# Optimization experiments

Hardware: AMD Instinct MI355X
Metric: run time of the kernel (lower is better)

The kernel has to match this reference:

```python
import jax, jax.numpy as jnp
import numpy as np

B, S, D, H = 2, 2048, 1024, 16
HD = D // H  # 64
ROPE_BASE = 10000.0


def _rope_tables(seq_len, head_dim):
    pos = jnp.arange(seq_len, dtype=jnp.float32)
    inv_freq = 1.0 / (ROPE_BASE ** (jnp.arange(0, head_dim, 2, dtype=jnp.float32) / head_dim))
    ang = pos[:, None] * inv_freq[None, :]            # [S, HD/2]
    emb = jnp.concatenate([ang, ang], axis=-1)        # [S, HD]
    return jnp.cos(emb), jnp.sin(emb)


def setup_inputs() -> dict:
    key = jax.random.key(0)
    k0, k1, k2 = jax.random.split(key, 3)
    x = jax.random.normal(k0, (B, S, D), dtype=jnp.float32)
    Wq = jax.random.normal(k1, (D, D), dtype=jnp.float32) * 0.02
    Wv = jax.random.normal(k2, (D, D), dtype=jnp.float32) * 0.02
    cos, sin = _rope_tables(S, HD)
    return {"x": x, "Wq": Wq, "Wv": Wv, "cos": cos, "sin": sin}


def _rotate_half(u):
    h = u.shape[-1] // 2
    return jnp.concatenate([-u[..., h:], u[..., :h]], axis=-1)


def reference(x, Wq, Wv, cos, sin):
    b, s, d = x.shape
    h, hd = H, d // H
    # NOTE: source module has xk = self.query(x) (key uses query weights) -- preserved.
    xq = (x @ Wq.T).reshape(b, s, h, hd)
    xk = (x @ Wq.T).reshape(b, s, h, hd)
    xv = (x @ Wv.T).reshape(b, s, h, hd)
    c = cos[None, :, None, :]  # [1,S,1,HD]
    sn = sin[None, :, None, :]
    q = xq * c + _rotate_half(xq) * sn
    k = xk * c + _rotate_half(xk) * sn
    q = q.transpose(0, 2, 1, 3)   # [B,H,S,HD]
    k = k.transpose(0, 2, 1, 3)
    v = xv.transpose(0, 2, 1, 3)
    scale = 1.0 / jnp.sqrt(jnp.asarray(hd, dtype=q.dtype))
    scores = jnp.einsum('bhqd,bhkd->bhqk', q, k) * scale  # [B,H,S,S]
    causal = jnp.tril(jnp.ones((s, s), dtype=bool))
    scores = jnp.where(causal[None, None, :, :], scores, jnp.finfo(scores.dtype).min)
    probs = jax.nn.softmax(scores, axis=-1)
    out = jnp.einsum('bhqk,bhkd->bhqd', probs, v)
    return out.transpose(0, 2, 1, 3).reshape(b, s, d)
```

## Files before the change

kernel.cpp:

```cpp
#include <hip/hip_runtime.h>


typedef float f32x4 __attribute__((ext_vector_type(4)));
typedef short s16x8 __attribute__((ext_vector_type(8)));

__device__ inline unsigned short f2bf(float f) {
  union { float f; unsigned u; } v; v.f = f;
  unsigned r = v.u + 0x7FFFu + ((v.u >> 16) & 1u);
  return (unsigned short)(r >> 16);
}

__device__ inline void gload16(const unsigned short* g, unsigned short* l) {
  __builtin_amdgcn_global_load_lds(
      (const __attribute__((address_space(1))) unsigned int*)g,
      (__attribute__((address_space(3))) unsigned int*)l, 16, 0, 0);
}

__global__ __launch_bounds__(256) void convert_all(
    const float* __restrict__ x, const float* __restrict__ wq,
    const float* __restrict__ wv, unsigned short* __restrict__ xb,
    unsigned short* __restrict__ wqb, unsigned short* __restrict__ wvb) {
  int i = blockIdx.x * 256 + threadIdx.x;
  const float* src; unsigned short* dst; int off;
  if (i < 1048576) { src = x; dst = xb; off = i; }
  else if (i < 1310720) { src = wq; dst = wqb; off = i - 1048576; }
  else { src = wv; dst = wvb; off = i - 1310720; }
  float4 v = ((const float4*)src)[off];
  ushort4 o;
  o.x = f2bf(v.x); o.y = f2bf(v.y); o.z = f2bf(v.z); o.w = f2bf(v.w);
  ((ushort4*)dst)[off] = o;
}

__global__ __launch_bounds__(256, 2) void qv_gemm(
    const unsigned short* __restrict__ A, const unsigned short* __restrict__ Wq,
    const unsigned short* __restrict__ Wv, const float* __restrict__ cosT,
    const float* __restrict__ sinT, unsigned short* __restrict__ Kf,
    unsigned short* __restrict__ Vf) {
  __shared__ unsigned short GS[2][2][128][64];
  int tid = threadIdx.x;
  int isq = blockIdx.x < 256;
  int b256 = blockIdx.x & 255;
  int bm = b256 & 31, bn = b256 >> 5;
  int w = tid >> 6, lane = tid & 63, lr = lane & 15, lg = lane >> 4;
  int wm = w >> 1, wn = w & 1;
  int l8 = lane >> 3, l7 = lane & 7;
  f32x4 acc[4][4] = {};

  const unsigned short* Wp = isq ? Wq : Wv;
  const unsigned short* srcbase =
      (w < 2) ? (A + bm * 128 * 1024) : (Wp + bn * 128 * 1024);
  int ab = w >> 1;

  auto stage = [&](int step) {
    int buf = step & 1, kt = step * 64;
#pragma unroll
    for (int i = 0; i < 8; ++i) {
      int rgrp = (w & 1) * 8 + i;
      int u = rgrp * 8 + l8;
      int ch = l7 ^ (u & 7);
      gload16(srcbase + u * 1024 + kt + ch * 8,
              (unsigned short*)&GS[buf][ab][rgrp * 8][0]);
    }
  };

  stage(0);
  for (int step = 0; step < 16; ++step) {
    int buf = step & 1;
    asm volatile("s_waitcnt vmcnt(0)" ::: "memory");
    __syncthreads();
    if (step + 1 < 16) stage(step + 1);
    s16x8 af[4][2], bfr[4][2];
#pragma unroll
    for (int mf = 0; mf < 4; ++mf)
#pragma unroll
      for (int kk = 0; kk < 2; ++kk)
        af[mf][kk] = *(const s16x8*)
            &GS[buf][0][wm * 64 + mf * 16 + lr][((kk * 4 + lg) ^ (lr & 7)) * 8];
#pragma unroll
    for (int nf = 0; nf < 4; ++nf)
#pragma unroll
      for (int kk = 0; kk < 2; ++kk)
        bfr[nf][kk] = *(const s16x8*)
            &GS[buf][1][wn * 64 + nf * 16 + lr][((kk * 4 + lg) ^ (lr & 7)) * 8];
#pragma unroll
    for (int mf = 0; mf < 4; ++mf)
#pragma unroll
      for (int nf = 0; nf < 4; ++nf)
#pragma unroll
        for (int kk = 0; kk < 2; ++kk)
          acc[mf][nf] = __builtin_amdgcn_mfma_f32_16x16x32_bf16(
              af[mf][kk], bfr[nf][kk], acc[mf][nf], 0, 0, 0);
  }

  int mBase = bm * 128 + wm * 64;
  int nBase = bn * 128 + wn * 64;
  if (isq) {
    __syncthreads();
    unsigned short* Lw = &GS[0][0][0][0] + w * (64 * 72);
    int wavebase = mBase;
    int bq = wavebase >> 11;
    int sbase = wavebase & 2047;
    int kt = sbase >> 6;
    int h = (nBase >> 6);
    int bh = bq * 16 + h;
#pragma unroll
    for (int mf = 0; mf < 4; ++mf)
#pragma unroll
      for (int j = 0; j < 4; ++j) {
        int sp = mf * 16 + 4 * lg + j;
        int s = sbase + sp;
#pragma unroll
        for (int nf = 0; nf < 4; ++nf) {
          int hd = nf * 16 + lr;
          float self = acc[mf][nf][j];
          float part = (nf < 2) ? -acc[mf][nf + 2][j] : acc[mf][nf - 2][j];
          float val = self * cosT[s * 64 + hd] + part * sinT[s * 64 + hd];
          Lw[sp * 72 + hd] = f2bf(val);
        }
      }
    asm volatile("s_waitcnt lgkmcnt(0)" ::: "memory");
    __builtin_amdgcn_sched_barrier(0);
    unsigned short* KfT = Kf + (size_t)(bh * 32 + kt) * 4096;
#pragma unroll
    for (int i = 0; i < 8; ++i) {
      int kk = i & 1, nfk = i >> 1;
      int lg2 = lane >> 4, lr2 = lane & 15;
      int sp = ((nfk >> 1) << 5) | ((lr2 >> 2) << 3) | ((nfk & 1) << 2) |
               (lr2 & 3);
      int c = kk * 4 + lg2;
      s16x8 vch = *(const s16x8*)&Lw[sp * 72 + c * 8];
      *(s16x8*)&KfT[(i * 64 + lane) * 8] = vch;
    }
  } else {
#pragma unroll
    for (int mf = 0; mf < 4; ++mf) {
      int m0 = mBase + mf * 16 + 4 * lg;
      int b = m0 >> 11, s0 = m0 & 2047;
      int kt = s0 >> 6, w0 = s0 & 63;
      int kkv = w0 >> 5, lg2 = (w0 >> 3) & 3, e0 = w0 & 7;
#pragma unroll
      for (int nf = 0; nf < 4; ++nf) {
        int col = nBase + nf * 16 + lr;
        int h = col >> 6;
        int bh = b * 16 + h;
        ushort4 pk;
        pk.x = f2bf(acc[mf][nf][0]); pk.y = f2bf(acc[mf][nf][1]);
        pk.z = f2bf(acc[mf][nf][2]); pk.w = f2bf(acc[mf][nf][3]);
        int idx = (((((bh * 32 + kt) * 4 + nf) * 2 + kkv) * 64) +
                   lg2 * 16 + lr) * 8 + e0;
        *(ushort4*)&Vf[idx] = pk;
      }
    }
  }
}

__global__ __launch_bounds__(256, 2) void attn(
    const unsigned short* __restrict__ Kf,
    const unsigned short* __restrict__ Vf,
    float* __restrict__ out) {
  __shared__ float MB[2][2][4][16][17];
  __shared__ float ML[2][2][2][16];
  const float SC = 0.125f * 1.44269504088896f;
  const float THR = 44.0f;
  int tid = threadIdx.x;
  int fid = blockIdx.x;
  int bh = 4 * (fid & 7) + ((fid >> 3) & 3);
  int qt = 31 - (fid >> 5);
  int w = tid >> 6, lane = tid & 63, lr = lane & 15, lg = lane >> 4;
  int q0 = qt * 64, qh = w >> 1, par = w & 1;

  const unsigned short* KfB = Kf + (size_t)bh * 32 * 4096;
  const unsigned short* VfB = Vf + (size_t)bh * 32 * 4096;

  s16x8 aq[2][2];
#pragma unroll
  for (int qs = 0; qs < 2; ++qs) {
    int qr = q0 + qh * 32 + 16 * qs + lr;
    int ktq = qr >> 6, w64 = qr & 63;
    int nfq = ((w64 >> 5) << 1) | ((w64 >> 2) & 1);
    int r31 = w64 & 31;
    int lr2 = ((r31 >> 3) << 2) | (r31 & 3);
#pragma unroll
    for (int kk = 0; kk < 2; ++kk)
      aq[qs][kk] = *(const s16x8*)
          &KfB[((((ktq * 4 + nfq) * 2 + kk) * 64) + lg * 16 + lr2) * 8];
  }

  f32x4 o[2][4] = {};
  float m_[2] = {-1e30f, -1e30f}, l_[2] = {0.f, 0.f};

  s16x8 kf[4][2], vf[4][2];
  auto loadK = [&](int kt) {
#pragma unroll
    for (int nf = 0; nf < 4; ++nf)
#pragma unroll
      for (int kk = 0; kk < 2; ++kk)
        kf[nf][kk] = *(const s16x8*)
            &KfB[(((kt * 4 + nf) * 2 + kk) * 64 + lane) * 8];
  };
  auto loadV = [&](int kt) {
#pragma unroll
    for (int nf = 0; nf < 4; ++nf)
#pragma unroll
      for (int kk = 0; kk < 2; ++kk)
        vf[nf][kk] = *(const s16x8*)
            &VfB[(((kt * 4 + nf) * 2 + kk) * 64 + lane) * 8];
  };

  int kt = par;
  bool active = kt <= qt;
  if (active) { loadK(kt); loadV(kt); }
  while (active) {
    f32x4 sa[2][4];
#pragma unroll
    for (int qs = 0; qs < 2; ++qs)
#pragma unroll
      for (int nf = 0; nf < 4; ++nf) sa[qs][nf] = (f32x4){0.f, 0.f, 0.f, 0.f};
#pragma unroll
    for (int kk = 0; kk < 2; ++kk)
#pragma unroll
      for (int nf = 0; nf < 4; ++nf)
#pragma unroll
        for (int qs = 0; qs < 2; ++qs)
          sa[qs][nf] = __builtin_amdgcn_mfma_f32_16x16x32_bf16(
              kf[nf][kk], aq[qs][kk], sa[qs][nf], 0, 0, 0);

    int ktn = kt + 2;
    bool more = ktn <= qt;
    if (more) loadK(ktn);

    if (kt == qt) {
#pragma unroll
      for (int qs = 0; qs < 2; ++qs) {
        int qglob = q0 + qh * 32 + 16 * qs + lr;
#pragma unroll
        for (int nf = 0; nf < 4; ++nf) {
          int kc = kt * 64 + 8 * lg + 4 * (nf & 1) + 32 * (nf >> 1);
#pragma unroll
          for (int j = 0; j < 4; ++j)
            if (kc + j > qglob) sa[qs][nf][j] = -3e38f;
        }
      }
    }
    float tm[2];
    float worst = -3e38f;
#pragma unroll
    for (int qs = 0; qs < 2; ++qs) {
      float t = sa[qs][0][0];
#pragma unroll
      for (int nf = 0; nf < 4; ++nf)
#pragma unroll
        for (int j = 0; j < 4; ++j) t = fmaxf(t, sa[qs][nf][j]);
      tm[qs] = t;
      worst = fmaxf(worst, t - m_[qs]);
    }
    if (!__all(worst <= THR)) {
#pragma unroll
      for (int qs = 0; qs < 2; ++qs) {
        float rm = fmaxf(tm[qs], __shfl_xor(tm[qs], 16));
        rm = fmaxf(rm, __shfl_xor(rm, 32));
        float mn = fmaxf(m_[qs], rm);
        float alpha = exp2f((m_[qs] - mn) * SC);
        m_[qs] = mn; l_[qs] *= alpha;
#pragma unroll
        for (int j = 0; j < 4; ++j) {
          float aj = __shfl(alpha, 4 * lg + j);
#pragma unroll
          for (int nf = 0; nf < 4; ++nf) o[qs][nf][j] *= aj;
        }
      }
    }
    unsigned cpk[2][8];
#pragma unroll
    for (int qs = 0; qs < 2; ++qs) {
      float msc = m_[qs] * SC;
#pragma unroll
      for (int nf = 0; nf < 4; ++nf) {
        float p0 = exp2f(fmaf(sa[qs][nf][0], SC, -msc));
        float p1 = exp2f(fmaf(sa[qs][nf][1], SC, -msc));
        float p2 = exp2f(fmaf(sa[qs][nf][2], SC, -msc));
        float p3 = exp2f(fmaf(sa[qs][nf][3], SC, -msc));
        l_[qs] += (p0 + p1) + (p2 + p3);
        unsigned r0, r1;
        asm("v_cvt_pk_bf16_f32 %0, %1, %2" : "=v"(r0) : "v"(p0), "v"(p1));
        asm("v_cvt_pk_bf16_f32 %0, %1, %2" : "=v"(r1) : "v"(p2), "v"(p3));
        cpk[qs][nf * 2] = r0; cpk[qs][nf * 2 + 1] = r1;
      }
    }
    s16x8 pav[2][2];
#pragma unroll
    for (int qs = 0; qs < 2; ++qs)
#pragma unroll
      for (int kk = 0; kk < 2; ++kk) {
        union { unsigned u[4]; s16x8 v; } pa;
        pa.u[0] = cpk[qs][4 * kk + 0]; pa.u[1] = cpk[qs][4 * kk + 1];
        pa.u[2] = cpk[qs][4 * kk + 2]; pa.u[3] = cpk[qs][4 * kk + 3];
        pav[qs][kk] = pa.v;
      }
#pragma unroll
    for (int kk = 0; kk < 2; ++kk)
#pragma unroll
      for (int nf = 0; nf < 4; ++nf)
#pragma unroll
        for (int qs = 0; qs < 2; ++qs)
          o[qs][nf] = __builtin_amdgcn_mfma_f32_16x16x32_bf16(
              pav[qs][kk], vf[nf][kk], o[qs][nf], 0, 0, 0);
    if (more) loadV(ktn);
    kt = ktn; active = more;
  }

#pragma unroll
  for (int qs = 0; qs < 2; ++qs) {
    float t = l_[qs];
    t += __shfl_xor(t, 16); t += __shfl_xor(t, 32);
    l_[qs] = t;
  }
  if (par) {
#pragma unroll
    for (int qs = 0; qs < 2; ++qs) {
#pragma unroll
      for (int nf = 0; nf < 4; ++nf)
#pragma unroll
        for (int j = 0; j < 4; ++j)
          MB[qh][qs][nf][4 * lg + j][lr] = o[qs][nf][j];
      if (lg == 0) {
        ML[qh][qs][0][lr] = m_[qs];
        ML[qh][qs][1][lr] = l_[qs];
      }
    }
  }
  __syncthreads();
  if (!par) {
    int b = bh >> 4, h = bh & 15;
#pragma unroll
    for (int qs = 0; qs < 2; ++qs) {
      float m1 = ML[qh][qs][0][lr];
      float l1 = ML[qh][qs][1][lr];
      float ms = fmaxf(m_[qs], m1);
      float a0 = exp2f((m_[qs] - ms) * SC), a1 = exp2f((m1 - ms) * SC);
      float inv = 1.0f / (a0 * l_[qs] + a1 * l1);
#pragma unroll
      for (int j = 0; j < 4; ++j) {
        float c0 = __shfl(a0 * inv, 4 * lg + j);
        float c1 = __shfl(a1 * inv, 4 * lg + j);
#pragma unroll
        for (int nf = 0; nf < 4; ++nf) {
          float o1 = MB[qh][qs][nf][4 * lg + j][lr];
          int q = q0 + qh * 32 + 16 * qs + 4 * lg + j;
          out[(b * 2048 + q) * 1024 + h * 64 + nf * 16 + lr] =
              c0 * o[qs][nf][j] + c1 * o1;
        }
      }
    }
  }
}

extern "C" void kernel_launch(void* const* d_in, const int* in_sizes, int n_in,
                              void* d_out, int out_size, void* d_ws, size_t ws_size,
                              hipStream_t stream) {
  const float* x = (const float*)d_in[0];
  const float* Wq = (const float*)d_in[1];
  const float* Wv = (const float*)d_in[2];
  const float* cosT = (const float*)d_in[3];
  const float* sinT = (const float*)d_in[4];
  float* out = (float*)d_out;

  unsigned short* xb = (unsigned short*)d_ws;
  unsigned short* wqb = xb + 4 * 1024 * 1024;
  unsigned short* wvb = wqb + 1024 * 1024;
  unsigned short* Kfb = wvb + 1024 * 1024;
  unsigned short* Vfb = Kfb + 4 * 1024 * 1024;

  convert_all<<<6144, 256, 0, stream>>>(x, Wq, Wv, xb, wqb, wvb);
  qv_gemm<<<512, 256, 0, stream>>>(xb, wqb, wvb, cosT, sinT, Kfb, Vfb);
  attn<<<1024, 256, 0, stream>>>(Kfb, Vfb, out);
}
```

Before: 66.09 us.

## Double attention query tile per block and interleave two QK/softmax groups

```diff
diff --git a/kernel.cpp b/kernel.cpp
--- a/kernel.cpp
+++ b/kernel.cpp
@@ -38,9 +38,11 @@
     unsigned short* __restrict__ Vf) {
   __shared__ unsigned short GS[2][2][128][64];
   int tid = threadIdx.x;
-  int isq = blockIdx.x < 256;
-  int b256 = blockIdx.x & 255;
-  int bm = b256 & 31, bn = b256 >> 5;
+  int fid = blockIdx.x;
+  int xcd = fid & 7, idx = fid >> 3;
+  int isq = idx & 1;
+  int bn = (idx >> 1) & 7;
+  int bm = xcd * 4 + (idx >> 4);
   int w = tid >> 6, lane = tid & 63, lr = lane & 15, lg = lane >> 4;
   int wm = w >> 1, wn = w & 1;
   int l8 = lane >> 3, l7 = lane & 7;
@@ -97,9 +99,8 @@
   if (isq) {
     __syncthreads();
     unsigned short* Lw = &GS[0][0][0][0] + w * (64 * 72);
-    int wavebase = mBase;
-    int bq = wavebase >> 11;
-    int sbase = wavebase & 2047;
+    int bq = mBase >> 11;
+    int sbase = mBase & 2047;
     int kt = sbase >> 6;
     int h = (nBase >> 6);
     int bh = bq * 16 + h;
@@ -146,9 +147,9 @@
         ushort4 pk;
         pk.x = f2bf(acc[mf][nf][0]); pk.y = f2bf(acc[mf][nf][1]);
         pk.z = f2bf(acc[mf][nf][2]); pk.w = f2bf(acc[mf][nf][3]);
-        int idx = (((((bh * 32 + kt) * 4 + nf) * 2 + kkv) * 64) +
-                   lg2 * 16 + lr) * 8 + e0;
-        *(ushort4*)&Vf[idx] = pk;
+        int idx2 = (((((bh * 32 + kt) * 4 + nf) * 2 + kkv) * 64) +
+                    lg2 * 16 + lr) * 8 + e0;
+        *(ushort4*)&Vf[idx2] = pk;
       }
     }
   }
@@ -158,24 +159,24 @@
     const unsigned short* __restrict__ Kf,
     const unsigned short* __restrict__ Vf,
     float* __restrict__ out) {
-  __shared__ float MB[2][2][4][16][17];
-  __shared__ float ML[2][2][2][16];
+  __shared__ float MB[2][4][4][16][17];
+  __shared__ float ML[2][4][2][16];
   const float SC = 0.125f * 1.44269504088896f;
   const float THR = 44.0f;
   int tid = threadIdx.x;
   int fid = blockIdx.x;
   int bh = 4 * (fid & 7) + ((fid >> 3) & 3);
-  int qt = 31 - (fid >> 5);
+  int qb = 15 - (fid >> 5);
   int w = tid >> 6, lane = tid & 63, lr = lane & 15, lg = lane >> 4;
-  int q0 = qt * 64, qh = w >> 1, par = w & 1;
+  int q0 = qb * 128, qh = w >> 1, par = w & 1;
 
   const unsigned short* KfB = Kf + (size_t)bh * 32 * 4096;
   const unsigned short* VfB = Vf + (size_t)bh * 32 * 4096;
 
-  s16x8 aq[2][2];
-#pragma unroll
-  for (int qs = 0; qs < 2; ++qs) {
-    int qr = q0 + qh * 32 + 16 * qs + lr;
+  s16x8 aq[4][2];
+#pragma unroll
+  for (int qs = 0; qs < 4; ++qs) {
+    int qr = q0 + qh * 64 + 16 * qs + lr;
     int ktq = qr >> 6, w64 = qr & 63;
     int nfq = ((w64 >> 5) << 1) | ((w64 >> 2) & 1);
     int r31 = w64 & 31;
@@ -186,8 +187,8 @@
           &KfB[((((ktq * 4 + nfq) * 2 + kk) * 64) + lg * 16 + lr2) * 8];
   }
 
-  f32x4 o[2][4] = {};
-  float m_[2] = {-1e30f, -1e30f}, l_[2] = {0.f, 0.f};
+  f32x4 o[4][4] = {};
+  float m_[4] = {-1e30f, -1e30f, -1e30f, -1e30f}, l_[4] = {0.f, 0.f, 0.f, 0.f};
 
   s16x8 kf[4][2], vf[4][2];
   auto loadK = [&](int kt) {
@@ -207,57 +208,56 @@
             &VfB[(((kt * 4 + nf) * 2 + kk) * 64 + lane) * 8];
   };
 
-  int kt = par;
-  bool active = kt <= qt;
-  if (active) { loadK(kt); loadV(kt); }
-  while (active) {
-    f32x4 sa[2][4];
-#pragma unroll
-    for (int qs = 0; qs < 2; ++qs)
-#pragma unroll
-      for (int nf = 0; nf < 4; ++nf) sa[qs][nf] = (f32x4){0.f, 0.f, 0.f, 0.f};
+  auto qk2 = [&](f32x4 (&sa)[2][4], int g) {
+#pragma unroll
+    for (int q2 = 0; q2 < 2; ++q2)
+#pragma unroll
+      for (int nf = 0; nf < 4; ++nf) sa[q2][nf] = (f32x4){0.f, 0.f, 0.f, 0.f};
+    __builtin_amdgcn_s_setprio(1);
 #pragma unroll
     for (int kk = 0; kk < 2; ++kk)
 #pragma unroll
       for (int nf = 0; nf < 4; ++nf)
 #pragma unroll
-        for (int qs = 0; qs < 2; ++qs)
-          sa[qs][nf] = __builtin_amdgcn_mfma_f32_16x16x32_bf16(
-              kf[nf][kk], aq[qs][kk], sa[qs][nf], 0, 0, 0);
-
-    int ktn = kt + 2;
-    bool more = ktn <= qt;
-    if (more) loadK(ktn);
-
-    if (kt == qt) {
-#pragma unroll
-      for (int qs = 0; qs < 2; ++qs) {
-        int qglob = q0 + qh * 32 + 16 * qs + lr;
-#pragma unroll
-        for (int nf = 0; nf < 4; ++nf) {
-          int kc = kt * 64 + 8 * lg + 4 * (nf & 1) + 32 * (nf >> 1);
-#pragma unroll
-          for (int j = 0; j < 4; ++j)
-            if (kc + j > qglob) sa[qs][nf][j] = -3e38f;
-        }
-      }
-    }
+        for (int q2 = 0; q2 < 2; ++q2)
+          sa[q2][nf] = __builtin_amdgcn_mfma_f32_16x16x32_bf16(
+              kf[nf][kk], aq[2 * g + q2][kk], sa[q2][nf], 0, 0, 0);
+    __builtin_amdgcn_s_setprio(0);
+  };
+
+  auto mask2 = [&](f32x4 (&sa)[2][4], int g, int kt) {
+#pragma unroll
+    for (int q2 = 0; q2 < 2; ++q2) {
+      int qglob = q0 + qh * 64 + 16 * (2 * g + q2) + lr;
+#pragma unroll
+      for (int nf = 0; nf < 4; ++nf) {
+        int kc = kt * 64 + 8 * lg + 4 * (nf & 1) + 32 * (nf >> 1);
+#pragma unroll
+        for (int j = 0; j < 4; ++j)
+          if (kc + j > qglob) sa[q2][nf][j] = -3e38f;
+      }
+    }
+  };
+
+  auto sm2 = [&](f32x4 (&sa)[2][4], int g, unsigned (&cpk)[2][8]) {
     float tm[2];
     float worst = -3e38f;
 #pragma unroll
-    for (int qs = 0; qs < 2; ++qs) {
-      float t = sa[qs][0][0];
+    for (int q2 = 0; q2 < 2; ++q2) {
+      int qs = 2 * g + q2;
+      float t = sa[q2][0][0];
 #pragma unroll
       for (int nf = 0; nf < 4; ++nf)
 #pragma unroll
-        for (int j = 0; j < 4; ++j) t = fmaxf(t, sa[qs][nf][j]);
-      tm[qs] = t;
+        for (int j = 0; j < 4; ++j) t = fmaxf(t, sa[q2][nf][j]);
+      tm[q2] = t;
       worst = fmaxf(worst, t - m_[qs]);
     }
     if (!__all(worst <= THR)) {
 #pragma unroll
-      for (int qs = 0; qs < 2; ++qs) {
-        float rm = fmaxf(tm[qs], __shfl_xor(tm[qs], 16));
+      for (int q2 = 0; q2 < 2; ++q2) {
+        int qs = 2 * g + q2;
+        float rm = fmaxf(tm[q2], __shfl_xor(tm[q2], 16));
         rm = fmaxf(rm, __shfl_xor(rm, 32));
         float mn = fmaxf(m_[qs], rm);
         float alpha = exp2f((m_[qs] - mn) * SC);
@@ -270,54 +270,76 @@
         }
       }
     }
-    unsigned cpk[2][8];
-#pragma unroll
-    for (int qs = 0; qs < 2; ++qs) {
+#pragma unroll
+    for (int q2 = 0; q2 < 2; ++q2) {
+      int qs = 2 * g + q2;
       float msc = m_[qs] * SC;
 #pragma unroll
       for (int nf = 0; nf < 4; ++nf) {
-        float p0 = exp2f(fmaf(sa[qs][nf][0], SC, -msc));
-        float p1 = exp2f(fmaf(sa[qs][nf][1], SC, -msc));
-        float p2 = exp2f(fmaf(sa[qs][nf][2], SC, -msc));
-        float p3 = exp2f(fmaf(sa[qs][nf][3], SC, -msc));
+        float p0 = exp2f(fmaf(sa[q2][nf][0], SC, -msc));
+        float p1 = exp2f(fmaf(sa[q2][nf][1], SC, -msc));
+        float p2 = exp2f(fmaf(sa[q2][nf][2], SC, -msc));
+        float p3 = exp2f(fmaf(sa[q2][nf][3], SC, -msc));
         l_[qs] += (p0 + p1) + (p2 + p3);
         unsigned r0, r1;
         asm("v_cvt_pk_bf16_f32 %0, %1, %2" : "=v"(r0) : "v"(p0), "v"(p1));
         asm("v_cvt_pk_bf16_f32 %0, %1, %2" : "=v"(r1) : "v"(p2), "v"(p3));
-        cpk[qs][nf * 2] = r0; cpk[qs][nf * 2 + 1] = r1;
-      }
-    }
-    s16x8 pav[2][2];
-#pragma unroll
-    for (int qs = 0; qs < 2; ++qs)
+        cpk[q2][nf * 2] = r0; cpk[q2][nf * 2 + 1] = r1;
+      }
+    }
+  };
+
+  auto pv2 = [&](unsigned (&cpk)[2][8], int g) {
+    __builtin_amdgcn_s_setprio(1);
+#pragma unroll
+    for (int q2 = 0; q2 < 2; ++q2) {
+      int qs = 2 * g + q2;
 #pragma unroll
       for (int kk = 0; kk < 2; ++kk) {
         union { unsigned u[4]; s16x8 v; } pa;
-        pa.u[0] = cpk[qs][4 * kk + 0]; pa.u[1] = cpk[qs][4 * kk + 1];
-        pa.u[2] = cpk[qs][4 * kk + 2]; pa.u[3] = cpk[qs][4 * kk + 3];
-        pav[qs][kk] = pa.v;
-      }
-#pragma unroll
-    for (int kk = 0; kk < 2; ++kk)
-#pragma unroll
-      for (int nf = 0; nf < 4; ++nf)
-#pragma unroll
-        for (int qs = 0; qs < 2; ++qs)
+        pa.u[0] = cpk[q2][4 * kk + 0]; pa.u[1] = cpk[q2][4 * kk + 1];
+        pa.u[2] = cpk[q2][4 * kk + 2]; pa.u[3] = cpk[q2][4 * kk + 3];
+#pragma unroll
+        for (int nf = 0; nf < 4; ++nf)
           o[qs][nf] = __builtin_amdgcn_mfma_f32_16x16x32_bf16(
-              pav[qs][kk], vf[nf][kk], o[qs][nf], 0, 0, 0);
+              pa.v, vf[nf][kk], o[qs][nf], 0, 0, 0);
+      }
+    }
+    __builtin_amdgcn_s_setprio(0);
+  };
+
+  int ktmax = 2 * qb + qh;
+  int kt = par;
+  bool active = kt <= ktmax;
+  if (active) { loadK(kt); loadV(kt); }
+  while (active) {
+    bool diag = (kt == ktmax);
+    f32x4 sa0[2][4], sa1[2][4];
+    unsigned cpk0[2][8], cpk1[2][8];
+    qk2(sa0, 0);
+    if (diag) mask2(sa0, 0, kt);
+    sm2(sa0, 0, cpk0);
+    qk2(sa1, 1);
+    int ktn = kt + 2;
+    bool more = ktn <= ktmax;
+    if (more) loadK(ktn);
+    if (diag) mask2(sa1, 1, kt);
+    sm2(sa1, 1, cpk1);
+    pv2(cpk0, 0);
+    pv2(cpk1, 1);
     if (more) loadV(ktn);
     kt = ktn; active = more;
   }
 
 #pragma unroll
-  for (int qs = 0; qs < 2; ++qs) {
+  for (int qs = 0; qs < 4; ++qs) {
     float t = l_[qs];
     t += __shfl_xor(t, 16); t += __shfl_xor(t, 32);
     l_[qs] = t;
   }
   if (par) {
 #pragma unroll
-    for (int qs = 0; qs < 2; ++qs) {
+    for (int qs = 0; qs < 4; ++qs) {
 #pragma unroll
       for (int nf = 0; nf < 4; ++nf)
 #pragma unroll
@@ -333,7 +355,7 @@
   if (!par) {
     int b = bh >> 4, h = bh & 15;
 #pragma unroll
-    for (int qs = 0; qs < 2; ++qs) {
+    for (int qs = 0; qs < 4; ++qs) {
       float m1 = ML[qh][qs][0][lr];
       float l1 = ML[qh][qs][1][lr];
       float ms = fmaxf(m_[qs], m1);
@@ -346,7 +368,7 @@
 #pragma unroll
         for (int nf = 0; nf < 4; ++nf) {
           float o1 = MB[qh][qs][nf][4 * lg + j][lr];
-          int q = q0 + qh * 32 + 16 * qs + 4 * lg + j;
+          int q = q0 + qh * 64 + 16 * qs + 4 * lg + j;
           out[(b * 2048 + q) * 1024 + h * 64 + nf * 16 + lr] =
               c0 * o[qs][nf][j] + c1 * o1;
         }
@@ -373,5 +395,5 @@
 
   convert_all<<<6144, 256, 0, stream>>>(x, Wq, Wv, xb, wqb, wvb);
   qv_gemm<<<512, 256, 0, stream>>>(xb, wqb, wvb, cosT, sinT, Kfb, Vfb);
-  attn<<<1024, 256, 0, stream>>>(Kfb, Vfb, out);
-}
+  attn<<<512, 256, 0, stream>>>(Kfb, Vfb, out);
+}
```

Result: slower. 93.66 us (+41.7%).

## Remap GEMM blocks per XCD, balance attention tile order, raise MFMA wave priority

Applied to the files above, without the earlier changes.

```diff
diff --git a/kernel.cpp b/kernel.cpp
--- a/kernel.cpp
+++ b/kernel.cpp
@@ -38,9 +38,11 @@
     unsigned short* __restrict__ Vf) {
   __shared__ unsigned short GS[2][2][128][64];
   int tid = threadIdx.x;
-  int isq = blockIdx.x < 256;
-  int b256 = blockIdx.x & 255;
-  int bm = b256 & 31, bn = b256 >> 5;
+  int fid = blockIdx.x;
+  int xcd = fid & 7, idx = fid >> 3;
+  int isq = idx & 1;
+  int bn = (idx >> 1) & 7;
+  int bm = xcd * 4 + (idx >> 4);
   int w = tid >> 6, lane = tid & 63, lr = lane & 15, lg = lane >> 4;
   int wm = w >> 1, wn = w & 1;
   int l8 = lane >> 3, l7 = lane & 7;
@@ -97,9 +99,8 @@
   if (isq) {
     __syncthreads();
     unsigned short* Lw = &GS[0][0][0][0] + w * (64 * 72);
-    int wavebase = mBase;
-    int bq = wavebase >> 11;
-    int sbase = wavebase & 2047;
+    int bq = mBase >> 11;
+    int sbase = mBase & 2047;
     int kt = sbase >> 6;
     int h = (nBase >> 6);
     int bh = bq * 16 + h;
@@ -146,9 +147,9 @@
         ushort4 pk;
         pk.x = f2bf(acc[mf][nf][0]); pk.y = f2bf(acc[mf][nf][1]);
         pk.z = f2bf(acc[mf][nf][2]); pk.w = f2bf(acc[mf][nf][3]);
-        int idx = (((((bh * 32 + kt) * 4 + nf) * 2 + kkv) * 64) +
-                   lg2 * 16 + lr) * 8 + e0;
-        *(ushort4*)&Vf[idx] = pk;
+        int idx2 = (((((bh * 32 + kt) * 4 + nf) * 2 + kkv) * 64) +
+                    lg2 * 16 + lr) * 8 + e0;
+        *(ushort4*)&Vf[idx2] = pk;
       }
     }
   }
@@ -165,7 +166,8 @@
   int tid = threadIdx.x;
   int fid = blockIdx.x;
   int bh = 4 * (fid & 7) + ((fid >> 3) & 3);
-  int qt = 31 - (fid >> 5);
+  int hi = fid >> 5;
+  int qt = (hi < 16) ? (31 - hi) : (hi - 16);
   int w = tid >> 6, lane = tid & 63, lr = lane & 15, lg = lane >> 4;
   int q0 = qt * 64, qh = w >> 1, par = w & 1;
 
@@ -190,21 +192,21 @@
   float m_[2] = {-1e30f, -1e30f}, l_[2] = {0.f, 0.f};
 
   s16x8 kf[4][2], vf[4][2];
-  auto loadK = [&](int kt) {
+  auto loadK = [&](int kt_) {
 #pragma unroll
     for (int nf = 0; nf < 4; ++nf)
 #pragma unroll
       for (int kk = 0; kk < 2; ++kk)
         kf[nf][kk] = *(const s16x8*)
-            &KfB[(((kt * 4 + nf) * 2 + kk) * 64 + lane) * 8];
+            &KfB[(((kt_ * 4 + nf) * 2 + kk) * 64 + lane) * 8];
   };
-  auto loadV = [&](int kt) {
+  auto loadV = [&](int kt_) {
 #pragma unroll
     for (int nf = 0; nf < 4; ++nf)
 #pragma unroll
       for (int kk = 0; kk < 2; ++kk)
         vf[nf][kk] = *(const s16x8*)
-            &VfB[(((kt * 4 + nf) * 2 + kk) * 64 + lane) * 8];
+            &VfB[(((kt_ * 4 + nf) * 2 + kk) * 64 + lane) * 8];
   };
 
   int kt = par;
@@ -216,6 +218,7 @@
     for (int qs = 0; qs < 2; ++qs)
 #pragma unroll
       for (int nf = 0; nf < 4; ++nf) sa[qs][nf] = (f32x4){0.f, 0.f, 0.f, 0.f};
+    __builtin_amdgcn_s_setprio(1);
 #pragma unroll
     for (int kk = 0; kk < 2; ++kk)
 #pragma unroll
@@ -224,6 +227,7 @@
         for (int qs = 0; qs < 2; ++qs)
           sa[qs][nf] = __builtin_amdgcn_mfma_f32_16x16x32_bf16(
               kf[nf][kk], aq[qs][kk], sa[qs][nf], 0, 0, 0);
+    __builtin_amdgcn_s_setprio(0);
 
     int ktn = kt + 2;
     bool more = ktn <= qt;
@@ -297,6 +301,7 @@
         pa.u[2] = cpk[qs][4 * kk + 2]; pa.u[3] = cpk[qs][4 * kk + 3];
         pav[qs][kk] = pa.v;
       }
+    __builtin_amdgcn_s_setprio(1);
 #pragma unroll
     for (int kk = 0; kk < 2; ++kk)
 #pragma unroll
@@ -305,6 +310,7 @@
         for (int qs = 0; qs < 2; ++qs)
           o[qs][nf] = __builtin_amdgcn_mfma_f32_16x16x32_bf16(
               pav[qs][kk], vf[nf][kk], o[qs][nf], 0, 0, 0);
+    __builtin_amdgcn_s_setprio(0);
     if (more) loadV(ktn);
     kt = ktn; active = more;
   }
```

Result: slower. 74.15 us (+12.2%).
